# Performance work log

Hardware: AMD Instinct MI355X
Metric: run time of the kernel (lower is better)

Reference implementation:

```python
import jax, jax.numpy as jnp
import numpy as np

ALPHA = 0.2  # LeakyReLU negative slope
NEG_INF = -9e15


def setup_inputs() -> dict:
    key = jax.random.key(0)
    k1, k2, k3, k4 = jax.random.split(key, 4)
    N, F = 1024, 64
    h = jax.random.normal(k1, (N, 2 * F), dtype=jnp.float32)
    adj = jax.random.normal(k2, (N, F), dtype=jnp.float32)
    # xavier_uniform-like scale for (2F, F) params, gain=1.414
    lim = 1.414 * np.sqrt(6.0 / (3 * F))
    W = jax.random.uniform(k3, (2 * F, F), dtype=jnp.float32, minval=-lim, maxval=lim)
    a = jax.random.uniform(k4, (2 * F, F), dtype=jnp.float32, minval=-lim, maxval=lim)
    return {"h": h, "adj": adj, "W": W, "a": a}


def reference(h, adj, W, a):
    F = W.shape[1]
    Wh = h @ W                                   # (N, F)
    # e[i,j,f] = leakyrelu(adj[i] @ a1 + adj[j] @ a2)[f] -- avoids (N,N,2F) concat
    s1 = adj @ a[:F]                             # (N, F) destination term
    s2 = adj @ a[F:]                             # (N, F) source term
    e = jax.nn.leaky_relu(s1[:, None, :] + s2[None, :, :], negative_slope=ALPHA)  # (N,N,F)
    # torch.where(adj > 0, e, -9e15): adj (N,F) broadcasts over dim 0 (source-node mask)
    att = jnp.where(adj[None, :, :] > 0, e, NEG_INF)
    attention_raw = jax.nn.softmax(att, axis=1)  # softmax over source nodes j
    # h_prime[i,f] = sum_j attention[i,j,f] * Wh[j,f]  (transpose+matmul+diagonal)
    h_prime = jnp.einsum('ijf,jf->if', attention_raw, Wh)
    return jax.nn.elu(h_prime), attention_raw
```

## Files before the change

kernel.cpp:

```cpp
#include <hip/hip_runtime.h>
#include <math.h>

#define GAT_ALPHA 0.2f

typedef float f32x4 __attribute__((ext_vector_type(4)));

__device__ __forceinline__ float lrelu_exp(float x) {
    float e = (x > 0.0f) ? x : (GAT_ALPHA * x);
    return __expf(e);
}

__global__ __launch_bounds__(256) void gat_prep(
    const float* __restrict__ h, const float* __restrict__ adj,
    const float* __restrict__ W, const float* __restrict__ a,
    float* __restrict__ Wh, float* __restrict__ s1, float* __restrict__ s2m)
{
    const int t = threadIdx.x;
    const int f = t & 63;
    const int i = (blockIdx.x << 2) + (t >> 6);

    const float* __restrict__ hrow = h + i * 128;
    const float* __restrict__ arow = adj + i * 64;

    float wh = 0.0f;
    #pragma unroll 8
    for (int k = 0; k < 128; ++k) wh = fmaf(hrow[k], W[k * 64 + f], wh);
    Wh[i * 64 + f] = wh;

    float v1 = 0.0f, v2 = 0.0f;
    #pragma unroll 8
    for (int k = 0; k < 64; ++k) {
        const float av = arow[k];
        v1 = fmaf(av, a[k * 64 + f], v1);
        v2 = fmaf(av, a[(64 + k) * 64 + f], v2);
    }
    s1[i * 64 + f] = v1;
    s2m[i * 64 + f] = (arow[f] > 0.0f) ? v2 : -1e30f;
}

__global__ __launch_bounds__(256) void gat_attn(
    const float* __restrict__ s1g, const float* __restrict__ s2m,
    const float* __restrict__ Wh,
    float* __restrict__ out_hp, float* __restrict__ out_att)
{
    __shared__ float red[16][64];
    __shared__ float zinv[64];

    const int t  = threadIdx.x;
    const int fg = t & 15;
    const int jo = t >> 4;
    const int i  = blockIdx.x;
    const int fb = fg << 2;

    const f32x4 s1v = *reinterpret_cast<const f32x4*>(s1g + i * 64 + fb);

    float z0 = 0.f, z1 = 0.f, z2 = 0.f, z3 = 0.f;
    #pragma unroll 2
    for (int jb = 0; jb < 1024; jb += 16) {
        const int j = jb + jo;
        const f32x4 sv = *reinterpret_cast<const f32x4*>(s2m + j * 64 + fb);
        z0 += lrelu_exp(s1v.x + sv.x);
        z1 += lrelu_exp(s1v.y + sv.y);
        z2 += lrelu_exp(s1v.z + sv.z);
        z3 += lrelu_exp(s1v.w + sv.w);
    }
    {
        f32x4 zp; zp.x = z0; zp.y = z1; zp.z = z2; zp.w = z3;
        *reinterpret_cast<f32x4*>(&red[jo][fb]) = zp;
    }
    __syncthreads();
    if (t < 64) {
        float z = 0.0f;
        #pragma unroll
        for (int o = 0; o < 16; ++o) z += red[o][t];
        zinv[t] = 1.0f / z;
    }
    __syncthreads();
    const f32x4 iv = *reinterpret_cast<const f32x4*>(&zinv[fb]);

    float h0 = 0.f, h1 = 0.f, h2 = 0.f, h3 = 0.f;
    float* __restrict__ arow_out = out_att + (size_t)i * 65536;
    #pragma unroll 2
    for (int jb = 0; jb < 1024; jb += 16) {
        const int j = jb + jo;
        const f32x4 sv = *reinterpret_cast<const f32x4*>(s2m + j * 64 + fb);
        const f32x4 wv = *reinterpret_cast<const f32x4*>(Wh + j * 64 + fb);
        f32x4 o;
        o.x = lrelu_exp(s1v.x + sv.x) * iv.x;
        o.y = lrelu_exp(s1v.y + sv.y) * iv.y;
        o.z = lrelu_exp(s1v.z + sv.z) * iv.z;
        o.w = lrelu_exp(s1v.w + sv.w) * iv.w;
        h0 = fmaf(o.x, wv.x, h0);
        h1 = fmaf(o.y, wv.y, h1);
        h2 = fmaf(o.z, wv.z, h2);
        h3 = fmaf(o.w, wv.w, h3);
        __builtin_nontemporal_store(o, reinterpret_cast<f32x4*>(arow_out + j * 64 + fb));
    }

    {
        f32x4 hp; hp.x = h0; hp.y = h1; hp.z = h2; hp.w = h3;
        *reinterpret_cast<f32x4*>(&red[jo][fb]) = hp;
    }
    __syncthreads();
    if (t < 64) {
        float v = 0.0f;
        #pragma unroll
        for (int o = 0; o < 16; ++o) v += red[o][t];
        out_hp[i * 64 + t] = (v > 0.0f) ? v : expm1f(v);
    }
}

extern "C" void kernel_launch(void* const* d_in, const int* in_sizes, int n_in,
                              void* d_out, int out_size, void* d_ws, size_t ws_size,
                              hipStream_t stream) {
    const float* h   = (const float*)d_in[0];
    const float* adj = (const float*)d_in[1];
    const float* W   = (const float*)d_in[2];
    const float* a   = (const float*)d_in[3];

    float* ws  = (float*)d_ws;
    float* Wh  = ws;
    float* s1  = ws + 65536;
    float* s2m = ws + 131072;

    float* out     = (float*)d_out;
    float* out_hp  = out;
    float* out_att = out + 65536;

    gat_prep<<<256, 256, 0, stream>>>(h, adj, W, a, Wh, s1, s2m);
    gat_attn<<<1024, 256, 0, stream>>>(s1, s2m, Wh, out_hp, out_att);
}
```

Measured before the change: 299.2 us.

## Factor exp of LeakyReLU into precomputed per-node exponentials, two rows per block

Since exp(lrelu(x+y)) equals max(exp(x)exp(y), exp(0.2x)exp(0.2y)), the prep kernel now precomputes four exponential tables. The attention kernel then uses only multiplies and a max instead of an exp per element. Each block now handles two destination rows with 512 threads, so every source-row load is reused twice. The nontemporal store was swapped for a plain store. The kernel is bound by the 256 MB attention write, so the compute savings may matter little, and the products could underflow or overflow for extreme inputs.

```diff
diff --git a/kernel.cpp b/kernel.cpp
--- a/kernel.cpp
+++ b/kernel.cpp
@@ -1,19 +1,13 @@
 #include <hip/hip_runtime.h>
 #include <math.h>
 
-#define GAT_ALPHA 0.2f
-
 typedef float f32x4 __attribute__((ext_vector_type(4)));
-
-__device__ __forceinline__ float lrelu_exp(float x) {
-    float e = (x > 0.0f) ? x : (GAT_ALPHA * x);
-    return __expf(e);
-}
 
 __global__ __launch_bounds__(256) void gat_prep(
     const float* __restrict__ h, const float* __restrict__ adj,
     const float* __restrict__ W, const float* __restrict__ a,
-    float* __restrict__ Wh, float* __restrict__ s1, float* __restrict__ s2m)
+    float* __restrict__ Wh, float* __restrict__ EA1, float* __restrict__ EA2,
+    float* __restrict__ EB1, float* __restrict__ EB2)
 {
     const int t = threadIdx.x;
     const int f = t & 63;
@@ -34,79 +28,107 @@
         v1 = fmaf(av, a[k * 64 + f], v1);
         v2 = fmaf(av, a[(64 + k) * 64 + f], v2);
     }
-    s1[i * 64 + f] = v1;
-    s2m[i * 64 + f] = (arow[f] > 0.0f) ? v2 : -1e30f;
+    EA1[i * 64 + f] = __expf(v1);
+    EA2[i * 64 + f] = __expf(0.2f * v1);
+    const bool m = arow[f] > 0.0f;
+    EB1[i * 64 + f] = m ? __expf(v2) : 0.0f;
+    EB2[i * 64 + f] = m ? __expf(0.2f * v2) : 0.0f;
 }
 
-__global__ __launch_bounds__(256) void gat_attn(
-    const float* __restrict__ s1g, const float* __restrict__ s2m,
+__global__ __launch_bounds__(512, 4) void gat_attn(
+    const float* __restrict__ EA1, const float* __restrict__ EA2,
+    const float* __restrict__ EB1, const float* __restrict__ EB2,
     const float* __restrict__ Wh,
     float* __restrict__ out_hp, float* __restrict__ out_att)
 {
-    __shared__ float red[16][64];
-    __shared__ float zinv[64];
+    __shared__ float red[2][32][64];
+    __shared__ float zinv[2][64];
 
     const int t  = threadIdx.x;
     const int fg = t & 15;
     const int jo = t >> 4;
-    const int i  = blockIdx.x;
     const int fb = fg << 2;
+    const int i0 = blockIdx.x << 1;
 
-    const f32x4 s1v = *reinterpret_cast<const f32x4*>(s1g + i * 64 + fb);
+    const f32x4 a1r0 = *reinterpret_cast<const f32x4*>(EA1 + (i0 + 0) * 64 + fb);
+    const f32x4 a2r0 = *reinterpret_cast<const f32x4*>(EA2 + (i0 + 0) * 64 + fb);
+    const f32x4 a1r1 = *reinterpret_cast<const f32x4*>(EA1 + (i0 + 1) * 64 + fb);
+    const f32x4 a2r1 = *reinterpret_cast<const f32x4*>(EA2 + (i0 + 1) * 64 + fb);
 
-    float z0 = 0.f, z1 = 0.f, z2 = 0.f, z3 = 0.f;
-    #pragma unroll 2
-    for (int jb = 0; jb < 1024; jb += 16) {
+    f32x4 z0 = {0.f, 0.f, 0.f, 0.f};
+    f32x4 z1 = {0.f, 0.f, 0.f, 0.f};
+    #pragma unroll 4
+    for (int jb = 0; jb < 1024; jb += 32) {
         const int j = jb + jo;
-        const f32x4 sv = *reinterpret_cast<const f32x4*>(s2m + j * 64 + fb);
-        z0 += lrelu_exp(s1v.x + sv.x);
-        z1 += lrelu_exp(s1v.y + sv.y);
-        z2 += lrelu_exp(s1v.z + sv.z);
-        z3 += lrelu_exp(s1v.w + sv.w);
+        const f32x4 b1 = *reinterpret_cast<const f32x4*>(EB1 + j * 64 + fb);
+        const f32x4 b2 = *reinterpret_cast<const f32x4*>(EB2 + j * 64 + fb);
+        z0.x += fmaxf(a1r0.x * b1.x, a2r0.x * b2.x);
+        z0.y += fmaxf(a1r0.y * b1.y, a2r0.y * b2.y);
+        z0.z += fmaxf(a1r0.z * b1.z, a2r0.z * b2.z);
+        z0.w += fmaxf(a1r0.w * b1.w, a2r0.w * b2.w);
+        z1.x += fmaxf(a1r1.x * b1.x, a2r1.x * b2.x);
+        z1.y += fmaxf(a1r1.y * b1.y, a2r1.y * b2.y);
+        z1.z += fmaxf(a1r1.z * b1.z, a2r1.z * b2.z);
+        z1.w += fmaxf(a1r1.w * b1.w, a2r1.w * b2.w);
     }
-    {
-        f32x4 zp; zp.x = z0; zp.y = z1; zp.z = z2; zp.w = z3;
-        *reinterpret_cast<f32x4*>(&red[jo][fb]) = zp;
+    *reinterpret_cast<f32x4*>(&red[0][jo][fb]) = z0;
+    *reinterpret_cast<f32x4*>(&red[1][jo][fb]) = z1;
+    __syncthreads();
+    if (t < 128) {
+        const int r = t >> 6, f = t & 63;
+        float z = 0.0f;
+        #pragma unroll
+        for (int o = 0; o < 32; ++o) z += red[r][o][f];
+        zinv[r][f] = 1.0f / z;
     }
     __syncthreads();
-    if (t < 64) {
-        float z = 0.0f;
-        #pragma unroll
-        for (int o = 0; o < 16; ++o) z += red[o][t];
-        zinv[t] = 1.0f / z;
-    }
-    __syncthreads();
-    const f32x4 iv = *reinterpret_cast<const f32x4*>(&zinv[fb]);
 
-    float h0 = 0.f, h1 = 0.f, h2 = 0.f, h3 = 0.f;
-    float* __restrict__ arow_out = out_att + (size_t)i * 65536;
-    #pragma unroll 2
-    for (int jb = 0; jb < 1024; jb += 16) {
-        const int j = jb + jo;
-        const f32x4 sv = *reinterpret_cast<const f32x4*>(s2m + j * 64 + fb);
-        const f32x4 wv = *reinterpret_cast<const f32x4*>(Wh + j * 64 + fb);
-        f32x4 o;
-        o.x = lrelu_exp(s1v.x + sv.x) * iv.x;
-        o.y = lrelu_exp(s1v.y + sv.y) * iv.y;
-        o.z = lrelu_exp(s1v.z + sv.z) * iv.z;
-        o.w = lrelu_exp(s1v.w + sv.w) * iv.w;
-        h0 = fmaf(o.x, wv.x, h0);
-        h1 = fmaf(o.y, wv.y, h1);
-        h2 = fmaf(o.z, wv.z, h2);
-        h3 = fmaf(o.w, wv.w, h3);
-        __builtin_nontemporal_store(o, reinterpret_cast<f32x4*>(arow_out + j * 64 + fb));
+    f32x4 s1r0, s2r0, s1r1, s2r1;
+    {
+        const f32x4 v0 = *reinterpret_cast<const f32x4*>(&zinv[0][fb]);
+        const f32x4 v1 = *reinterpret_cast<const f32x4*>(&zinv[1][fb]);
+        s1r0.x = a1r0.x * v0.x; s1r0.y = a1r0.y * v0.y; s1r0.z = a1r0.z * v0.z; s1r0.w = a1r0.w * v0.w;
+        s2r0.x = a2r0.x * v0.x; s2r0.y = a2r0.y * v0.y; s2r0.z = a2r0.z * v0.z; s2r0.w = a2r0.w * v0.w;
+        s1r1.x = a1r1.x * v1.x; s1r1.y = a1r1.y * v1.y; s1r1.z = a1r1.z * v1.z; s1r1.w = a1r1.w * v1.w;
+        s2r1.x = a2r1.x * v1.x; s2r1.y = a2r1.y * v1.y; s2r1.z = a2r1.z * v1.z; s2r1.w = a2r1.w * v1.w;
     }
 
-    {
-        f32x4 hp; hp.x = h0; hp.y = h1; hp.z = h2; hp.w = h3;
-        *reinterpret_cast<f32x4*>(&red[jo][fb]) = hp;
+    f32x4 h0 = {0.f, 0.f, 0.f, 0.f};
+    f32x4 h1 = {0.f, 0.f, 0.f, 0.f};
+    float* __restrict__ o0 = out_att + (size_t)(i0 + 0) * 65536 + fb;
+    float* __restrict__ o1 = out_att + (size_t)(i0 + 1) * 65536 + fb;
+    #pragma unroll 4
+    for (int jb = 0; jb < 1024; jb += 32) {
+        const int j = jb + jo;
+        const f32x4 b1 = *reinterpret_cast<const f32x4*>(EB1 + j * 64 + fb);
+        const f32x4 b2 = *reinterpret_cast<const f32x4*>(EB2 + j * 64 + fb);
+        const f32x4 wv = *reinterpret_cast<const f32x4*>(Wh  + j * 64 + fb);
+        f32x4 oA, oB;
+        oA.x = fmaxf(s1r0.x * b1.x, s2r0.x * b2.x);
+        oA.y = fmaxf(s1r0.y * b1.y, s2r0.y * b2.y);
+        oA.z = fmaxf(s1r0.z * b1.z, s2r0.z * b2.z);
+        oA.w = fmaxf(s1r0.w * b1.w, s2r0.w * b2.w);
+        oB.x = fmaxf(s1r1.x * b1.x, s2r1.x * b2.x);
+        oB.y = fmaxf(s1r1.y * b1.y, s2r1.y * b2.y);
+        oB.z = fmaxf(s1r1.z * b1.z, s2r1.z * b2.z);
+        oB.w = fmaxf(s1r1.w * b1.w, s2r1.w * b2.w);
+        h0.x = fmaf(oA.x, wv.x, h0.x); h0.y = fmaf(oA.y, wv.y, h0.y);
+        h0.z = fmaf(oA.z, wv.z, h0.z); h0.w = fmaf(oA.w, wv.w, h0.w);
+        h1.x = fmaf(oB.x, wv.x, h1.x); h1.y = fmaf(oB.y, wv.y, h1.y);
+        h1.z = fmaf(oB.z, wv.z, h1.z); h1.w = fmaf(oB.w, wv.w, h1.w);
+        *reinterpret_cast<f32x4*>(o0 + j * 64) = oA;
+        *reinterpret_cast<f32x4*>(o1 + j * 64) = oB;
     }
+
+    *reinterpret_cast<f32x4*>(&red[0][jo][fb]) = h0;
+    *reinterpret_cast<f32x4*>(&red[1][jo][fb]) = h1;
     __syncthreads();
-    if (t < 64) {
+    if (t < 128) {
+        const int r = t >> 6, f = t & 63;
         float v = 0.0f;
         #pragma unroll
-        for (int o = 0; o < 16; ++o) v += red[o][t];
-        out_hp[i * 64 + t] = (v > 0.0f) ? v : expm1f(v);
+        for (int o = 0; o < 32; ++o) v += red[r][o][f];
+        out_hp[(i0 + r) * 64 + f] = (v > 0.0f) ? v : expm1f(v);
     }
 }
 
@@ -120,13 +142,15 @@
 
     float* ws  = (float*)d_ws;
     float* Wh  = ws;
-    float* s1  = ws + 65536;
-    float* s2m = ws + 131072;
+    float* EA1 = ws + 65536;
+    float* EA2 = ws + 131072;
+    float* EB1 = ws + 196608;
+    float* EB2 = ws + 262144;
 
     float* out     = (float*)d_out;
     float* out_hp  = out;
     float* out_att = out + 65536;
 
-    gat_prep<<<256, 256, 0, stream>>>(h, adj, W, a, Wh, s1, s2m);
-    gat_attn<<<1024, 256, 0, stream>>>(s1, s2m, Wh, out_hp, out_att);
+    gat_prep<<<256, 256, 0, stream>>>(h, adj, W, a, Wh, EA1, EA2, EB1, EB2);
+    gat_attn<<<512, 512, 0, stream>>>(EA1, EA2, EB1, EB2, Wh, out_hp, out_att);
 }
```

New measurement: 314.8 us. 5.2% more time.

## Factor exp(leakyrelu) into precomputed exponentials and split attention write kernel

Applied to the files above, without the earlier changes.

Uses exp(lrelu(x+y)) = max(e^x e^y, e^{0.2x} e^{0.2y}) to precompute per-node exponentials in the prep kernel, which removes every exp from the N*N*F loops. Normalizer and h_prime are now computed in one pass by a new kernel that writes zinv. A separate 1024-thread kernel writes the attention tensor four rows at a time with prefetched source vectors. The risks are overflow or underflow of the unshifted exponentials, an extra kernel launch, and plain stores where nontemporal stores were used before.

```diff
diff --git a/kernel.cpp b/kernel.cpp
--- a/kernel.cpp
+++ b/kernel.cpp
@@ -1,19 +1,13 @@
 #include <hip/hip_runtime.h>
 #include <math.h>
 
-#define GAT_ALPHA 0.2f
-
 typedef float f32x4 __attribute__((ext_vector_type(4)));
-
-__device__ __forceinline__ float lrelu_exp(float x) {
-    float e = (x > 0.0f) ? x : (GAT_ALPHA * x);
-    return __expf(e);
-}
 
 __global__ __launch_bounds__(256) void gat_prep(
     const float* __restrict__ h, const float* __restrict__ adj,
     const float* __restrict__ W, const float* __restrict__ a,
-    float* __restrict__ Wh, float* __restrict__ s1, float* __restrict__ s2m)
+    float* __restrict__ Wh, float* __restrict__ EA1, float* __restrict__ EA2,
+    float* __restrict__ EB1, float* __restrict__ EB2)
 {
     const int t = threadIdx.x;
     const int f = t & 63;
@@ -34,79 +28,127 @@
         v1 = fmaf(av, a[k * 64 + f], v1);
         v2 = fmaf(av, a[(64 + k) * 64 + f], v2);
     }
-    s1[i * 64 + f] = v1;
-    s2m[i * 64 + f] = (arow[f] > 0.0f) ? v2 : -1e30f;
+    EA1[i * 64 + f] = __expf(v1);
+    EA2[i * 64 + f] = __expf(0.2f * v1);
+    const bool m = arow[f] > 0.0f;
+    EB1[i * 64 + f] = m ? __expf(v2) : 0.0f;
+    EB2[i * 64 + f] = m ? __expf(0.2f * v2) : 0.0f;
 }
 
-__global__ __launch_bounds__(256) void gat_attn(
-    const float* __restrict__ s1g, const float* __restrict__ s2m,
+__global__ __launch_bounds__(256) void gat_zh(
+    const float* __restrict__ EA1, const float* __restrict__ EA2,
+    const float* __restrict__ EB1, const float* __restrict__ EB2,
     const float* __restrict__ Wh,
-    float* __restrict__ out_hp, float* __restrict__ out_att)
+    float* __restrict__ zinv_g, float* __restrict__ out_hp)
 {
-    __shared__ float red[16][64];
-    __shared__ float zinv[64];
+    __shared__ float redz[16][64];
+    __shared__ float redh[16][64];
 
     const int t  = threadIdx.x;
     const int fg = t & 15;
     const int jo = t >> 4;
+    const int fb = fg << 2;
     const int i  = blockIdx.x;
-    const int fb = fg << 2;
 
-    const f32x4 s1v = *reinterpret_cast<const f32x4*>(s1g + i * 64 + fb);
+    const f32x4 a1 = *reinterpret_cast<const f32x4*>(EA1 + i * 64 + fb);
+    const f32x4 a2 = *reinterpret_cast<const f32x4*>(EA2 + i * 64 + fb);
 
-    float z0 = 0.f, z1 = 0.f, z2 = 0.f, z3 = 0.f;
-    #pragma unroll 2
+    f32x4 z  = {0.f, 0.f, 0.f, 0.f};
+    f32x4 hv = {0.f, 0.f, 0.f, 0.f};
+    #pragma unroll 4
     for (int jb = 0; jb < 1024; jb += 16) {
         const int j = jb + jo;
-        const f32x4 sv = *reinterpret_cast<const f32x4*>(s2m + j * 64 + fb);
-        z0 += lrelu_exp(s1v.x + sv.x);
-        z1 += lrelu_exp(s1v.y + sv.y);
-        z2 += lrelu_exp(s1v.z + sv.z);
-        z3 += lrelu_exp(s1v.w + sv.w);
+        const f32x4 b1 = *reinterpret_cast<const f32x4*>(EB1 + j * 64 + fb);
+        const f32x4 b2 = *reinterpret_cast<const f32x4*>(EB2 + j * 64 + fb);
+        const f32x4 wv = *reinterpret_cast<const f32x4*>(Wh  + j * 64 + fb);
+        f32x4 e;
+        e.x = fmaxf(a1.x * b1.x, a2.x * b2.x);
+        e.y = fmaxf(a1.y * b1.y, a2.y * b2.y);
+        e.z = fmaxf(a1.z * b1.z, a2.z * b2.z);
+        e.w = fmaxf(a1.w * b1.w, a2.w * b2.w);
+        z.x += e.x; z.y += e.y; z.z += e.z; z.w += e.w;
+        hv.x = fmaf(e.x, wv.x, hv.x);
+        hv.y = fmaf(e.y, wv.y, hv.y);
+        hv.z = fmaf(e.z, wv.z, hv.z);
+        hv.w = fmaf(e.w, wv.w, hv.w);
     }
-    {
-        f32x4 zp; zp.x = z0; zp.y = z1; zp.z = z2; zp.w = z3;
-        *reinterpret_cast<f32x4*>(&red[jo][fb]) = zp;
-    }
+    *reinterpret_cast<f32x4*>(&redz[jo][fb]) = z;
+    *reinterpret_cast<f32x4*>(&redh[jo][fb]) = hv;
     __syncthreads();
     if (t < 64) {
-        float z = 0.0f;
+        float zs = 0.0f, hs = 0.0f;
         #pragma unroll
-        for (int o = 0; o < 16; ++o) z += red[o][t];
-        zinv[t] = 1.0f / z;
+        for (int o = 0; o < 16; ++o) { zs += redz[o][t]; hs += redh[o][t]; }
+        const float iv = 1.0f / zs;
+        zinv_g[i * 64 + t] = iv;
+        const float v = hs * iv;
+        out_hp[i * 64 + t] = (v > 0.0f) ? v : expm1f(v);
     }
-    __syncthreads();
-    const f32x4 iv = *reinterpret_cast<const f32x4*>(&zinv[fb]);
+}
 
-    float h0 = 0.f, h1 = 0.f, h2 = 0.f, h3 = 0.f;
-    float* __restrict__ arow_out = out_att + (size_t)i * 65536;
-    #pragma unroll 2
-    for (int jb = 0; jb < 1024; jb += 16) {
-        const int j = jb + jo;
-        const f32x4 sv = *reinterpret_cast<const f32x4*>(s2m + j * 64 + fb);
-        const f32x4 wv = *reinterpret_cast<const f32x4*>(Wh + j * 64 + fb);
-        f32x4 o;
-        o.x = lrelu_exp(s1v.x + sv.x) * iv.x;
-        o.y = lrelu_exp(s1v.y + sv.y) * iv.y;
-        o.z = lrelu_exp(s1v.z + sv.z) * iv.z;
-        o.w = lrelu_exp(s1v.w + sv.w) * iv.w;
-        h0 = fmaf(o.x, wv.x, h0);
-        h1 = fmaf(o.y, wv.y, h1);
-        h2 = fmaf(o.z, wv.z, h2);
-        h3 = fmaf(o.w, wv.w, h3);
-        __builtin_nontemporal_store(o, reinterpret_cast<f32x4*>(arow_out + j * 64 + fb));
+__global__ __launch_bounds__(1024) void gat_att(
+    const float* __restrict__ EA1, const float* __restrict__ EA2,
+    const float* __restrict__ EB1, const float* __restrict__ EB2,
+    const float* __restrict__ zinv_g,
+    float* __restrict__ out_att)
+{
+    const int t  = threadIdx.x;
+    const int fg = t & 15;
+    const int jo = t >> 4;
+    const int fb = fg << 2;
+    const int i0 = blockIdx.x << 2;
+
+    f32x4 s1[4], s2[4];
+    #pragma unroll
+    for (int r = 0; r < 4; ++r) {
+        const f32x4 a1 = *reinterpret_cast<const f32x4*>(EA1 + (i0 + r) * 64 + fb);
+        const f32x4 a2 = *reinterpret_cast<const f32x4*>(EA2 + (i0 + r) * 64 + fb);
+        const f32x4 iv = *reinterpret_cast<const f32x4*>(zinv_g + (i0 + r) * 64 + fb);
+        s1[r].x = a1.x * iv.x; s1[r].y = a1.y * iv.y; s1[r].z = a1.z * iv.z; s1[r].w = a1.w * iv.w;
+        s2[r].x = a2.x * iv.x; s2[r].y = a2.y * iv.y; s2[r].z = a2.z * iv.z; s2[r].w = a2.w * iv.w;
     }
 
-    {
-        f32x4 hp; hp.x = h0; hp.y = h1; hp.z = h2; hp.w = h3;
-        *reinterpret_cast<f32x4*>(&red[jo][fb]) = hp;
-    }
-    __syncthreads();
-    if (t < 64) {
-        float v = 0.0f;
-        #pragma unroll
-        for (int o = 0; o < 16; ++o) v += red[o][t];
-        out_hp[i * 64 + t] = (v > 0.0f) ? v : expm1f(v);
+    const int jbase = jo * 64 + fb;
+    float* __restrict__ o0 = out_att + (size_t)i0 * 65536 + fb;
+
+    f32x4 b1A = *reinterpret_cast<const f32x4*>(EB1 + jbase);
+    f32x4 b2A = *reinterpret_cast<const f32x4*>(EB2 + jbase);
+    f32x4 b1B = *reinterpret_cast<const f32x4*>(EB1 + jbase + 64 * 64);
+    f32x4 b2B = *reinterpret_cast<const f32x4*>(EB2 + jbase + 64 * 64);
+
+    for (int jb = 0; jb < 1024; jb += 128) {
+        {
+            f32x4 o_[4];
+            #pragma unroll
+            for (int r = 0; r < 4; ++r) {
+                o_[r].x = fmaxf(s1[r].x * b1A.x, s2[r].x * b2A.x);
+                o_[r].y = fmaxf(s1[r].y * b1A.y, s2[r].y * b2A.y);
+                o_[r].z = fmaxf(s1[r].z * b1A.z, s2[r].z * b2A.z);
+                o_[r].w = fmaxf(s1[r].w * b1A.w, s2[r].w * b2A.w);
+            }
+            const int jp = (jb + 128) & 1023;
+            b1A = *reinterpret_cast<const f32x4*>(EB1 + jp * 64 + jbase);
+            b2A = *reinterpret_cast<const f32x4*>(EB2 + jp * 64 + jbase);
+            #pragma unroll
+            for (int r = 0; r < 4; ++r)
+                *reinterpret_cast<f32x4*>(o0 + r * 65536 + jb * 64 + jo * 64) = o_[r];
+        }
+        {
+            f32x4 o_[4];
+            #pragma unroll
+            for (int r = 0; r < 4; ++r) {
+                o_[r].x = fmaxf(s1[r].x * b1B.x, s2[r].x * b2B.x);
+                o_[r].y = fmaxf(s1[r].y * b1B.y, s2[r].y * b2B.y);
+                o_[r].z = fmaxf(s1[r].z * b1B.z, s2[r].z * b2B.z);
+                o_[r].w = fmaxf(s1[r].w * b1B.w, s2[r].w * b2B.w);
+            }
+            const int jp = (jb + 192) & 1023;
+            b1B = *reinterpret_cast<const f32x4*>(EB1 + jp * 64 + jbase);
+            b2B = *reinterpret_cast<const f32x4*>(EB2 + jp * 64 + jbase);
+            #pragma unroll
+            for (int r = 0; r < 4; ++r)
+                *reinterpret_cast<f32x4*>(o0 + r * 65536 + (jb + 64) * 64 + jo * 64) = o_[r];
+        }
     }
 }
 
@@ -118,15 +160,19 @@
     const float* W   = (const float*)d_in[2];
     const float* a   = (const float*)d_in[3];
 
-    float* ws  = (float*)d_ws;
-    float* Wh  = ws;
-    float* s1  = ws + 65536;
-    float* s2m = ws + 131072;
+    float* ws   = (float*)d_ws;
+    float* Wh   = ws;
+    float* EA1  = ws + 65536;
+    float* EA2  = ws + 131072;
+    float* EB1  = ws + 196608;
+    float* EB2  = ws + 262144;
+    float* zinv = ws + 327680;
 
     float* out     = (float*)d_out;
     float* out_hp  = out;
     float* out_att = out + 65536;
 
-    gat_prep<<<256, 256, 0, stream>>>(h, adj, W, a, Wh, s1, s2m);
-    gat_attn<<<1024, 256, 0, stream>>>(s1, s2m, Wh, out_hp, out_att);
+    gat_prep<<<256, 256, 0, stream>>>(h, adj, W, a, Wh, EA1, EA2, EB1, EB2);
+    gat_zh<<<1024, 256, 0, stream>>>(EA1, EA2, EB1, EB2, Wh, zinv, out_hp);
+    gat_att<<<256, 1024, 0, stream>>>(EA1, EA2, EB1, EB2, zinv, out_att);
 }
```

Result: no change. 298.3 us (-0.3%).
